# Performance work log

Measured on AMD Instinct MI355X. Metric: run time of the kernel, lower is better.

## Reference

```python
import jax, jax.numpy as jnp
import numpy as np

UP = 2
NUM_POINT = 9
GROUPS = 4


def pixel_shuffle(t, r):
    # [B, C*r*r, H, W] -> [B, C, H*r, W*r], torch layout: in[b, c*r*r + i*r + j, h, w] -> out[b, c, h*r+i, w*r+j]
    B, C, H, W = t.shape
    Co = C // (r * r)
    t = t.reshape(B, Co, r, r, H, W)
    t = t.transpose(0, 1, 4, 2, 5, 3)
    return t.reshape(B, Co, H * r, W * r)


def _bilinear_sample(feat, py, px):
    # feat: [E, H, W]; py, px: [P, Hup, Wup] in low-res pixel coords (zero padding outside)
    H, W = feat.shape[1], feat.shape[2]
    y0f = jnp.floor(py)
    x0f = jnp.floor(px)
    ty = py - y0f
    tx = px - x0f
    y0 = y0f.astype(jnp.int32)
    x0 = x0f.astype(jnp.int32)
    out = jnp.zeros(feat.shape[:1] + py.shape, dtype=feat.dtype)
    corners = ((0, 0, (1 - ty) * (1 - tx)), (0, 1, (1 - ty) * tx),
               (1, 0, ty * (1 - tx)), (1, 1, ty * tx))
    for dy, dx, w in corners:
        yi = y0 + dy
        xi = x0 + dx
        valid = ((yi >= 0) & (yi < H) & (xi >= 0) & (xi < W)).astype(feat.dtype)
        yc = jnp.clip(yi, 0, H - 1)
        xc = jnp.clip(xi, 0, W - 1)
        out = out + feat[:, yc, xc] * (w * valid)[None]
    return out  # [E, P, Hup, Wup]

# vmap over batch and group dims
_sample_bg = jax.vmap(jax.vmap(_bilinear_sample))


def setup_inputs() -> dict:
    key = jax.random.key(0)
    ks = jax.random.split(key, 8)
    B, Cy, Cx = 2, 256, 256
    H, W = 64, 64
    Hup, Wup = H * UP, W * UP
    GE = GROUPS * 32              # q/k channels = groups * embedding_dim
    OFF = GROUPS * NUM_POINT * 2 * UP * UP  # 288
    return {
        "y": jax.random.normal(ks[0], (B, Cy, Hup, Wup), jnp.float32),
        "x": jax.random.normal(ks[1], (B, Cx, H, W), jnp.float32),
        "Wq": jax.random.normal(ks[2], (GE, Cy), jnp.float32) * 0.02,
        "bq": jnp.zeros((GE,), jnp.float32),
        "Wk": jax.random.normal(ks[3], (GE, Cx), jnp.float32) * 0.02,
        "bk": jnp.zeros((GE,), jnp.float32),
        "Woff": jax.random.normal(ks[4], (OFF, Cx), jnp.float32) * 0.02,
        "boff": jnp.zeros((OFF,), jnp.float32),
    }


def reference(y, x, Wq, bq, Wk, bk, Woff, boff):
    G, P, up = GROUPS, NUM_POINT, UP
    B, C, H, W = x.shape
    # 1x1 convs as einsum
    q = jnp.einsum('oi,bihw->bohw', Wq, y) + bq[None, :, None, None]
    k = jnp.einsum('oi,bihw->bohw', Wk, x) + bk[None, :, None, None]
    off = jnp.einsum('oi,bihw->bohw', Woff, x) + boff[None, :, None, None]
    off = pixel_shuffle(off, up)  # [B, G*P*2, Hup, Wup]
    Hup, Wup = off.shape[2], off.shape[3]
    off = off.reshape(B, G, P, 2, Hup, Wup)
    # sampling positions in low-res coordinates: align-centers base + learned offset
    base_y = (jnp.arange(Hup, dtype=jnp.float32) + 0.5) / up - 0.5
    base_x = (jnp.arange(Wup, dtype=jnp.float32) + 0.5) / up - 0.5
    py = off[:, :, :, 0] + base_y[None, None, None, :, None]  # [B,G,P,Hup,Wup]
    px = off[:, :, :, 1] + base_x[None, None, None, None, :]
    E = Wq.shape[0] // G
    qg = q.reshape(B, G, E, Hup, Wup)
    kg = k.reshape(B, G, E, H, W)
    # deform_qk: gather k at offset points, dot with q over embedding dim
    ks = _sample_bg(kg, py, px)                    # [B,G,E,P,Hup,Wup]
    attn = jnp.einsum('bgehw,bgephw->bgphw', qg, ks)
    attn = jax.nn.softmax(attn, axis=2)            # softmax over points
    # deform_av: gather x at the same points, weighted sum by attn
    Cg = C // G
    xg = x.reshape(B, G, Cg, H, W)
    xs = _sample_bg(xg, py, px)                    # [B,G,Cg,P,Hup,Wup]
    out = jnp.einsum('bgphw,bgcphw->bgchw', attn, xs)
    return out.reshape(B, C, Hup, Wup)
```

## Files before the change

### kernel.cpp

```cpp
#include <hip/hip_runtime.h>

#define B_N   2
#define H_LR  64
#define W_LR  64
#define HUP   128
#define WUP   128
#define GRP   4
#define NPT   9
#define EMB   32
#define CGRP  64
#define KIN   256
#define GE    128
#define NOFF  288

typedef __attribute__((ext_vector_type(8))) short short8v;
typedef _Float16 half8v __attribute__((ext_vector_type(8)));
typedef __attribute__((ext_vector_type(4))) float f32x4;

__device__ __forceinline__ ushort f2bf(float f) {
    unsigned u = __float_as_uint(f);
    u += 0x7FFFu + ((u >> 16) & 1u);
    return (ushort)(u >> 16);
}
__device__ __forceinline__ float bf2f(ushort h) {
    return __uint_as_float(((unsigned)h) << 16);
}
__device__ __forceinline__ ushort f2h(float f) {
    _Float16 h = (_Float16)f;
    return __builtin_bit_cast(ushort, h);
}
__device__ __forceinline__ float h2f(ushort u) {
    _Float16 h = __builtin_bit_cast(_Float16, u);
    return (float)h;
}

__global__ __launch_bounds__(256) void convert_w_kernel(
    const float* __restrict__ Wq, const float* __restrict__ Wk,
    const float* __restrict__ Woff, ushort* __restrict__ wqbf,
    ushort* __restrict__ wkobf)
{
    int r = blockIdx.x, k = threadIdx.x;
    if (r < 128) {
        wqbf[r * 256 + k] = f2bf(Wq[r * 256 + k]);
    } else {
        int r2 = r - 128;
        float v = 0.f;
        if (r2 < 128) v = Wk[r2 * 256 + k];
        else if (r2 < 416) v = Woff[(r2 - 128) * 256 + k];
        wkobf[r2 * 256 + k] = f2bf(v);
    }
}

__global__ __launch_bounds__(256, 4) void mfma_gemm(
    const float* __restrict__ y, const float* __restrict__ x,
    const ushort* __restrict__ WQ, const ushort* __restrict__ WKO,
    const float* __restrict__ bq, const float* __restrict__ bk,
    const float* __restrict__ boff,
    ushort* __restrict__ qbf, ushort* __restrict__ kbf,
    float* __restrict__ offw)
{
    __shared__ __align__(16) ushort sY[64][68];
    __shared__ __align__(16) ushort sB[128][72];

    int bid = blockIdx.x;
    const float* SRC; const ushort* WBF; const float* ba; const float* bb;
    ushort* OBF; float* OFP;
    int M, m0, n0, b;
    if (bid < 512) {
        int mt = bid & 255; b = bid >> 8;
        SRC = y; WBF = WQ; ba = bq; bb = nullptr; OBF = qbf; OFP = nullptr;
        M = 16384; m0 = mt * 64; n0 = 0;
    } else {
        int r = bid - 512;
        int mt = r & 63, nt2 = (r >> 6) & 3; b = r >> 8;
        SRC = x; WBF = WKO; ba = bk; bb = boff; OBF = kbf; OFP = offw;
        M = 4096; m0 = mt * 64; n0 = nt2 * 128;
    }

    int tid = threadIdx.x;
    int lane = tid & 63;
    int wv = tid >> 6, wm = wv >> 1, wn = wv & 1;
    int il = lane & 15, g4 = lane >> 4;
    int st_m4 = tid & 15, st_c = tid >> 4;
    int st_c8 = tid & 7,  st_n = tid >> 3;

    f32x4 acc[2][4];
#pragma unroll
    for (int i = 0; i < 2; ++i)
#pragma unroll
        for (int j = 0; j < 4; ++j) { f32x4 z = {0.f,0.f,0.f,0.f}; acc[i][j] = z; }

    const float* src_b = SRC + (size_t)b * KIN * M;

    float4 ra[4]; short8v rb[4];
#pragma unroll
    for (int i = 0; i < 4; ++i)
        ra[i] = *(const float4*)&src_b[(size_t)(st_c + i * 16) * M + m0 + st_m4 * 4];
#pragma unroll
    for (int i = 0; i < 4; ++i)
        rb[i] = *(const short8v*)&WBF[(size_t)(n0 + st_n + i * 32) * KIN + st_c8 * 8];

    for (int ks = 0; ks < 4; ++ks) {
#pragma unroll
        for (int i = 0; i < 4; ++i) {
            ushort4 h;
            h.x = f2bf(ra[i].x); h.y = f2bf(ra[i].y);
            h.z = f2bf(ra[i].z); h.w = f2bf(ra[i].w);
            *(ushort4*)&sY[st_c + i * 16][st_m4 * 4] = h;
            *(short8v*)&sB[st_n + i * 32][st_c8 * 8] = rb[i];
        }
        __syncthreads();
        if (ks < 3) {
            int k0 = (ks + 1) * 64;
#pragma unroll
            for (int i = 0; i < 4; ++i)
                ra[i] = *(const float4*)&src_b[(size_t)(k0 + st_c + i * 16) * M + m0 + st_m4 * 4];
#pragma unroll
            for (int i = 0; i < 4; ++i)
                rb[i] = *(const short8v*)&WBF[(size_t)(n0 + st_n + i * 32) * KIN + k0 + st_c8 * 8];
        }
#pragma unroll
        for (int kc = 0; kc < 2; ++kc) {
            int kb = kc * 32 + g4 * 8;
            short8v af[2], bfr[4];
#pragma unroll
            for (int mf = 0; mf < 2; ++mf) {
                int m = wm * 32 + mf * 16 + il;
                short8v t;
#pragma unroll
                for (int j = 0; j < 8; ++j) t[j] = (short)sY[kb + j][m];
                af[mf] = t;
            }
#pragma unroll
            for (int nf = 0; nf < 4; ++nf)
                bfr[nf] = *(const short8v*)&sB[wn * 64 + nf * 16 + il][kb];
#pragma unroll
            for (int mf = 0; mf < 2; ++mf)
#pragma unroll
                for (int nf = 0; nf < 4; ++nf)
                    acc[mf][nf] = __builtin_amdgcn_mfma_f32_16x16x32_bf16(
                        af[mf], bfr[nf], acc[mf][nf], 0, 0, 0);
        }
        __syncthreads();
    }

#pragma unroll
    for (int mf = 0; mf < 2; ++mf) {
#pragma unroll
        for (int r = 0; r < 4; ++r) {
            int m = m0 + wm * 32 + mf * 16 + g4 * 4 + r;
            size_t row = (size_t)b * M + m;
#pragma unroll
            for (int nf = 0; nf < 4; ++nf) {
                int n = n0 + wn * 64 + nf * 16 + il;
                float v = acc[mf][nf][r];
                if (n < GE) {
                    OBF[row * 128 + n] = f2bf(v + ba[n]);
                } else {
                    int no = n - GE;
                    if (no < NOFF) OFP[row * 288 + no] = v + bb[no];
                }
            }
        }
    }
}

#define RROWS 6
#define RCOLS 11
#define RPX   66

__global__ __launch_bounds__(256, 4) void deform_kernel(
    const ushort* __restrict__ qbf,
    const ushort* __restrict__ kbf,
    const float* __restrict__ offw,
    const float* __restrict__ x,
    float* __restrict__ out)
{
    __shared__ __align__(16) char smem[36272];
    ushort (*sXt)[72] = (ushort(*)[72])(smem);
    ushort (*sK)[40]  = (ushort(*)[40])(smem + 9216);
    ushort (*sQ)[40]  = (ushort(*)[40])(smem + 14496);
    ushort (*sSW)[72] = (ushort(*)[72])(smem + 19616);
    uint*  sGt        = (uint*)(smem + 28832);
    int*   sGz        = (int*)(smem + 31136);
    float* sAttn      = (float*)(smem + 33440);
    int*   sFB        = (int*)(smem + 35744);
    float (*sOT)[76]  = (float(*)[76])(smem);
    float* sOff       = (float*)(smem + 19616);

    int bx = blockIdx.x;
    int tw = bx & 7, th = (bx >> 3) & 31, g = (bx >> 8) & 3, b = bx >> 10;
    int tid = threadIdx.x;
    int wv_ = tid >> 6, lane = tid & 63;
    int row = lane & 15, kb8 = lane >> 4;

    const int ry0 = th * 2 - 2, rx0 = tw * 8 - 1;

    if (tid == 0) sFB[0] = 0;
    if (tid < 192) {
        int r = tid / 3, c2 = tid - (tid / 3) * 3;
        *(uint*)&sXt[r][66 + c2 * 2] = 0;
    }
    for (int it = tid; it < 1536; it += 256) {
        int quad = it & 3, rest = it >> 2;
        int ch = rest / 6, gy = rest - (rest / 6) * 6;
        int gyg = min(max(ry0 + gy, 0), 63);
        const float* xr = x + ((size_t)b * 256 + g * CGRP + ch) * 4096 + gyg * 64;
        if (tw >= 1 && tw <= 6) {
            float4 f = *(const float4*)&xr[rx0 - 3 + quad * 4];
            const float* fv = (const float*)&f;
#pragma unroll
            for (int j = 0; j < 4; ++j) {
                int col = quad * 4 + j - 3;
                if (col >= 0 && col < RCOLS) sXt[ch][gy * RCOLS + col] = f2h(fv[j]);
            }
        } else {
#pragma unroll
            for (int j = 0; j < 4; ++j) {
                int col = quad * 4 + j - 3;
                if (col >= 0 && col < RCOLS) {
                    int gxg = min(max(rx0 + col, 0), 63);
                    sXt[ch][gy * RCOLS + col] = f2h(xr[gxg]);
                }
            }
        }
    }
    for (int i = tid; i < 264; i += 256) {
        int rp = i >> 2, c4 = i & 3;
        int qy = rp / RCOLS, qx = rp - qy * RCOLS;
        int gy = min(max(ry0 + qy, 0), 63), gx = min(max(rx0 + qx, 0), 63);
        *(short8v*)&sK[rp][c4 * 8] =
            *(const short8v*)&kbf[((size_t)b * 4096 + gy * 64 + gx) * 128 +
                                  g * EMB + c4 * 8];
    }
    {
        int px = tid >> 2, c4 = tid & 3;
        int hup = th * 4 + (px >> 4), wup = tw * 16 + (px & 15);
        *(short8v*)&sQ[px][c4 * 8] =
            *(const short8v*)&qbf[((size_t)b * 16384 + hup * 128 + wup) * 128 +
                                  g * EMB + c4 * 8];
    }
    for (int i = tid; i < 288; i += 256) {
        int lr = i / 18, f4 = i - (i / 18) * 18;
        int yy = th * 2 + (lr >> 3), xx = tw * 8 + (lr & 7);
        *(float4*)&sOff[lr * 72 + f4 * 4] =
            *(const float4*)&offw[((size_t)b * 4096 + yy * 64 + xx) * 288 +
                                  g * 72 + f4 * 4];
    }
    __syncthreads();

    f32x4 sreg[5];
    {
        short8v a = *(const short8v*)&sQ[wv_ * 16 + row][kb8 * 8];
#pragma unroll
        for (int nt = 0; nt < 5; ++nt) {
            int rr = nt * 16 + row; if (rr > 65) rr = 65;
            short8v bf = *(const short8v*)&sK[rr][kb8 * 8];
            f32x4 z = {0.f, 0.f, 0.f, 0.f};
            sreg[nt] = __builtin_amdgcn_mfma_f32_16x16x32_bf16(a, bf, z, 0, 0, 0);
        }
    }
    for (int item = tid; item < 576; item += 256) {
        int px = item / 9, pt = item - (item / 9) * 9;
        int lx = px & 15, ly = px >> 4;
        int hup = th * 4 + ly, wup = tw * 16 + lx;
        int lr = (ly >> 1) * 8 + (lx >> 1);
        int ij = ((hup & 1) << 1) | (wup & 1);
        float offy = sOff[lr * 72 + pt * 8 + ij];
        float offx = sOff[lr * 72 + pt * 8 + 4 + ij];
        float py  = offy + hup * 0.5f - 0.25f;
        float pxx = offx + wup * 0.5f - 0.25f;
        float y0f = floorf(py), x0f = floorf(pxx);
        float ty = py - y0f, tx = pxx - x0f;
        int y0 = (int)y0f, x0 = (int)x0f;
        int mk = 0;
        if ((unsigned)y0 < 64u && (unsigned)x0 < 64u)         mk |= 1;
        if ((unsigned)y0 < 64u && (unsigned)(x0+1) < 64u)     mk |= 2;
        if ((unsigned)(y0+1) < 64u && (unsigned)x0 < 64u)     mk |= 4;
        if ((unsigned)(y0+1) < 64u && (unsigned)(x0+1) < 64u) mk |= 8;
        int iy = y0 - ry0, ix = x0 - rx0;
        bool inreg = ((unsigned)iy <= (unsigned)(RROWS - 2)) &&
                     ((unsigned)ix <= (unsigned)(RCOLS - 2));
        int fl, zp;
        if (!mk)        { fl = 16; zp = 0; }
        else if (inreg) { fl = mk | 16; zp = iy * RCOLS + ix; }
        else            { fl = mk; zp = (y0 + 1) * 66 + (x0 + 1); }
        sGt[item] = (uint)f2h(ty) | ((uint)f2h(tx) << 16);
        sGz[item] = (zp << 5) | fl;
    }
    __syncthreads();

#pragma unroll
    for (int nt = 0; nt < 5; ++nt) {
        int rp = nt * 16 + row;
        if (rp < RPX) {
#pragma unroll
            for (int r = 0; r < 4; ++r)
                sSW[wv_ * 16 + kb8 * 4 + r][rp] = f2h(sreg[nt][r]);
        }
    }
    __syncthreads();

    for (int item = tid; item < 576; item += 256) {
        int px = item / 9;
        uint gt = sGt[item];
        float ty = h2f((ushort)gt), tx = h2f((ushort)(gt >> 16));
        int z = sGz[item];
        int fl = z & 31;
        float a;
        if (fl & 16) {
            int zi = z >> 5;
            float w00 = (1.f - ty) * (1.f - tx), w01 = (1.f - ty) * tx;
            float w10 = ty * (1.f - tx), w11 = ty * tx;
            a  = (fl & 1) ? w00 * h2f(sSW[px][zi])             : 0.f;
            a += (fl & 2) ? w01 * h2f(sSW[px][zi + 1])         : 0.f;
            a += (fl & 4) ? w10 * h2f(sSW[px][zi + RCOLS])     : 0.f;
            a += (fl & 8) ? w11 * h2f(sSW[px][zi + RCOLS + 1]) : 0.f;
        } else {
            int t = z >> 5;
            int y0 = t / 66 - 1, x0 = t - (t / 66) * 66 - 1;
            a = 0.f;
#pragma unroll
            for (int c = 0; c < 4; ++c) if ((fl >> c) & 1) {
                int dy = c >> 1, dx = c & 1;
                float wgt = (dy ? ty : 1.f - ty) * (dx ? tx : 1.f - tx);
                const ushort* kr = &kbf[((size_t)b * 4096 + (y0 + dy) * 64 + x0 + dx) * 128 +
                                        g * EMB];
                float dot = 0.f;
                for (int e = 0; e < EMB; ++e) dot += bf2f(sQ[px][e]) * bf2f(kr[e]);
                a += wgt * dot;
            }
            int old = atomicAdd(&sFB[0], 1);
            if (old < 128) sFB[1 + old] = item;
        }
        sAttn[item] = a;
    }
    __syncthreads();

    if (tid < 64) {
        float aa[NPT];
        float mx = -1e30f;
#pragma unroll
        for (int p = 0; p < NPT; ++p) { aa[p] = sAttn[tid * 9 + p]; mx = fmaxf(mx, aa[p]); }
        float s = 0.f;
#pragma unroll
        for (int p = 0; p < NPT; ++p) { aa[p] = __expf(aa[p] - mx); s += aa[p]; }
        float inv = 1.f / s;
#pragma unroll
        for (int p = 0; p < NPT; ++p) sAttn[tid * 9 + p] = aa[p] * inv;
    } else {
        float4* p = (float4*)&sSW[0][0];
        float4 z4 = make_float4(0.f, 0.f, 0.f, 0.f);
        for (int i = tid - 64; i < 576; i += 192) p[i] = z4;
    }
    __syncthreads();

    if (tid < 64) {
        int px = tid;
#pragma unroll
        for (int pt = 0; pt < NPT; ++pt) {
            int item = px * 9 + pt;
            int z = sGz[item];
            int fl = z & 31;
            if (!(fl & 16)) continue;
            uint gt = sGt[item];
            float ty = h2f((ushort)gt), tx = h2f((ushort)(gt >> 16));
            float a = sAttn[item];
            int zi = z >> 5;
            ushort* c = &sSW[px][zi];
            if (fl & 1) c[0]         = f2h(h2f(c[0])         + (1.f-ty)*(1.f-tx)*a);
            if (fl & 2) c[1]         = f2h(h2f(c[1])         + (1.f-ty)*tx*a);
            if (fl & 4) c[RCOLS]     = f2h(h2f(c[RCOLS])     + ty*(1.f-tx)*a);
            if (fl & 8) c[RCOLS + 1] = f2h(h2f(c[RCOLS + 1]) + ty*tx*a);
        }
    }
    __syncthreads();

    f32x4 oacc[4];
    {
        half8v bfm0[4], bfm1[4], bfm2[4];
#pragma unroll
        for (int nt = 0; nt < 4; ++nt) {
            bfm0[nt] = *(const half8v*)&sXt[nt * 16 + row][kb8 * 8];
            bfm1[nt] = *(const half8v*)&sXt[nt * 16 + row][32 + kb8 * 8];
            bfm2[nt] = *(const half8v*)&sXt[nt * 16 + row][64];
        }
        int px = wv_ * 16 + row;
        half8v af0 = *(const half8v*)&sSW[px][kb8 * 8];
        half8v af1 = *(const half8v*)&sSW[px][32 + kb8 * 8];
        half8v af2 = {0,0,0,0,0,0,0,0};
        if (kb8 == 0) af2 = *(const half8v*)&sSW[px][64];

#pragma unroll
        for (int nt = 0; nt < 4; ++nt) { f32x4 z = {0.f,0.f,0.f,0.f}; oacc[nt] = z; }
#pragma unroll
        for (int nt = 0; nt < 4; ++nt) {
            oacc[nt] = __builtin_amdgcn_mfma_f32_16x16x32_f16(af0, bfm0[nt], oacc[nt], 0, 0, 0);
            oacc[nt] = __builtin_amdgcn_mfma_f32_16x16x32_f16(af1, bfm1[nt], oacc[nt], 0, 0, 0);
            oacc[nt] = __builtin_amdgcn_mfma_f32_16x16x32_f16(af2, bfm2[nt], oacc[nt], 0, 0, 0);
        }
    }
    __syncthreads();

#pragma unroll
    for (int nt = 0; nt < 4; ++nt)
        *(f32x4*)&sOT[nt * 16 + row][wv_ * 16 + kb8 * 4] = oacc[nt];
    __syncthreads();

    {
#pragma unroll
        for (int i = 0; i < 4; ++i) {
            int pr = i * 64 + (tid >> 2);
            int ch = pr >> 2, hupl = pr & 3, q = tid & 3;
            float4 v = *(float4*)&sOT[ch][hupl * 16 + q * 4];
            *(float4*)(out + ((size_t)b * 256 + g * CGRP + ch) * 16384 +
                       (size_t)(th * 4 + hupl) * 128 + tw * 16 + q * 4) = v;
        }
    }
    __syncthreads();

    int nfb = min(sFB[0], 128);
    for (int i = 0; i < nfb; ++i) {
        if (tid < 64) {
            int item = sFB[1 + i];
            int px = item / 9;
            uint gt = sGt[item];
            float ty = h2f((ushort)gt), tx = h2f((ushort)(gt >> 16));
            int z = sGz[item];
            float a = sAttn[item];
            int fl = z & 15;
            int t = z >> 5;
            int y0 = t / 66 - 1, x0 = t - (t / 66) * 66 - 1;
            const float* xg = x + ((size_t)b * 256 + g * CGRP + tid) * 4096;
            float v = 0.f;
            if (fl & 1) v += (1.f-ty)*(1.f-tx)*a * xg[y0*64 + x0];
            if (fl & 2) v += (1.f-ty)*tx*a       * xg[y0*64 + x0 + 1];
            if (fl & 4) v += ty*(1.f-tx)*a       * xg[(y0+1)*64 + x0];
            if (fl & 8) v += ty*tx*a             * xg[(y0+1)*64 + x0 + 1];
            int hup = th * 4 + (px >> 4), wup = tw * 16 + (px & 15);
            float* op = out + ((size_t)b * 256 + g * CGRP + tid) * 16384 +
                        hup * 128 + wup;
            *op += v;
        }
    }
}

extern "C" void kernel_launch(void* const* d_in, const int* in_sizes, int n_in,
                              void* d_out, int out_size, void* d_ws, size_t ws_size,
                              hipStream_t stream)
{
    const float* y    = (const float*)d_in[0];
    const float* x    = (const float*)d_in[1];
    const float* Wq   = (const float*)d_in[2];
    const float* bq   = (const float*)d_in[3];
    const float* Wk   = (const float*)d_in[4];
    const float* bk   = (const float*)d_in[5];
    const float* Woff = (const float*)d_in[6];
    const float* boff = (const float*)d_in[7];
    float* out = (float*)d_out;

    ushort* wqbf  = (ushort*)d_ws;
    ushort* wkobf = wqbf + 128 * 256;
    ushort* qbf   = wkobf + 512 * 256;
    ushort* kbf   = qbf + (size_t)B_N * 16384 * 128;
    float*  offw  = (float*)(kbf + (size_t)B_N * 4096 * 128);

    convert_w_kernel<<<dim3(640), dim3(256), 0, stream>>>(Wq, Wk, Woff, wqbf, wkobf);

    mfma_gemm<<<dim3(1024), dim3(256), 0, stream>>>(
        y, x, wqbf, wkobf, bq, bk, boff, qbf, kbf, offw);

    deform_kernel<<<dim3(2048), dim3(256), 0, stream>>>(qbf, kbf, offw, x, out);
}
```

Before: 71.37 us.

## Fuse attention gather, softmax and scatter into one per-pixel pass

The deform kernel now writes the QK MFMA scores straight to shared memory instead of holding them in registers. One thread per pixel then gathers the scores, runs the softmax and scatters the bilinear weights in a single pass. This removes the separate attention buffer and several block barriers, and the fallback list now stores the softmax weight with each item. The final barrier is skipped when no out-of-region samples occur. In exchange, the attention work runs on one wave instead of all four, and the fallback list capacity drops from 128 to 64 entries.

```diff
diff --git a/kernel.cpp b/kernel.cpp
--- a/kernel.cpp
+++ b/kernel.cpp
@@ -176,17 +176,17 @@
     const float* __restrict__ x,
     float* __restrict__ out)
 {
-    __shared__ __align__(16) char smem[36272];
+    __shared__ __align__(16) char smem[37808];
     ushort (*sXt)[72] = (ushort(*)[72])(smem);
-    ushort (*sK)[40]  = (ushort(*)[40])(smem + 9216);
-    ushort (*sQ)[40]  = (ushort(*)[40])(smem + 14496);
-    ushort (*sSW)[72] = (ushort(*)[72])(smem + 19616);
-    uint*  sGt        = (uint*)(smem + 28832);
-    int*   sGz        = (int*)(smem + 31136);
-    float* sAttn      = (float*)(smem + 33440);
-    int*   sFB        = (int*)(smem + 35744);
-    float (*sOT)[76]  = (float(*)[76])(smem);
-    float* sOff       = (float*)(smem + 19616);
+    ushort (*sS)[66]  = (ushort(*)[66])(smem + 9216);
+    uint*  sGt        = (uint*)(smem + 17664);
+    int*   sGz        = (int*)(smem + 19968);
+    int*   sFB        = (int*)(smem + 22272);
+    ushort (*sQ)[40]  = (ushort(*)[40])(smem + 22800);
+    ushort (*sK)[40]  = (ushort(*)[40])(smem + 27920);
+    float* sOff       = (float*)(smem + 33200);
+    ushort (*sW)[72]  = (ushort(*)[72])(smem + 27920);
+    float (*sOT)[68]  = (float(*)[68])(smem);
 
     int bx = blockIdx.x;
     int tw = bx & 7, th = (bx >> 3) & 31, g = (bx >> 8) & 3, b = bx >> 10;
@@ -249,7 +249,6 @@
     }
     __syncthreads();
 
-    f32x4 sreg[5];
     {
         short8v a = *(const short8v*)&sQ[wv_ * 16 + row][kb8 * 8];
 #pragma unroll
@@ -257,7 +256,13 @@
             int rr = nt * 16 + row; if (rr > 65) rr = 65;
             short8v bf = *(const short8v*)&sK[rr][kb8 * 8];
             f32x4 z = {0.f, 0.f, 0.f, 0.f};
-            sreg[nt] = __builtin_amdgcn_mfma_f32_16x16x32_bf16(a, bf, z, 0, 0, 0);
+            f32x4 d = __builtin_amdgcn_mfma_f32_16x16x32_bf16(a, bf, z, 0, 0, 0);
+            int rp = nt * 16 + row;
+            if (rp < RPX) {
+#pragma unroll
+                for (int r = 0; r < 4; ++r)
+                    sS[wv_ * 16 + kb8 * 4 + r][rp] = f2h(d[r]);
+            }
         }
     }
     for (int item = tid; item < 576; item += 256) {
@@ -290,88 +295,81 @@
     }
     __syncthreads();
 
-#pragma unroll
-    for (int nt = 0; nt < 5; ++nt) {
-        int rp = nt * 16 + row;
-        if (rp < RPX) {
-#pragma unroll
-            for (int r = 0; r < 4; ++r)
-                sSW[wv_ * 16 + kb8 * 4 + r][rp] = f2h(sreg[nt][r]);
-        }
-    }
-    __syncthreads();
-
-    for (int item = tid; item < 576; item += 256) {
-        int px = item / 9;
-        uint gt = sGt[item];
-        float ty = h2f((ushort)gt), tx = h2f((ushort)(gt >> 16));
-        int z = sGz[item];
-        int fl = z & 31;
-        float a;
-        if (fl & 16) {
-            int zi = z >> 5;
-            float w00 = (1.f - ty) * (1.f - tx), w01 = (1.f - ty) * tx;
-            float w10 = ty * (1.f - tx), w11 = ty * tx;
-            a  = (fl & 1) ? w00 * h2f(sSW[px][zi])             : 0.f;
-            a += (fl & 2) ? w01 * h2f(sSW[px][zi + 1])         : 0.f;
-            a += (fl & 4) ? w10 * h2f(sSW[px][zi + RCOLS])     : 0.f;
-            a += (fl & 8) ? w11 * h2f(sSW[px][zi + RCOLS + 1]) : 0.f;
-        } else {
-            int t = z >> 5;
-            int y0 = t / 66 - 1, x0 = t - (t / 66) * 66 - 1;
-            a = 0.f;
-#pragma unroll
-            for (int c = 0; c < 4; ++c) if ((fl >> c) & 1) {
-                int dy = c >> 1, dx = c & 1;
-                float wgt = (dy ? ty : 1.f - ty) * (dx ? tx : 1.f - tx);
-                const ushort* kr = &kbf[((size_t)b * 4096 + (y0 + dy) * 64 + x0 + dx) * 128 +
-                                        g * EMB];
-                float dot = 0.f;
-                for (int e = 0; e < EMB; ++e) dot += bf2f(sQ[px][e]) * bf2f(kr[e]);
-                a += wgt * dot;
-            }
-            int old = atomicAdd(&sFB[0], 1);
-            if (old < 128) sFB[1 + old] = item;
-        }
-        sAttn[item] = a;
-    }
-    __syncthreads();
-
     if (tid < 64) {
-        float aa[NPT];
-        float mx = -1e30f;
-#pragma unroll
-        for (int p = 0; p < NPT; ++p) { aa[p] = sAttn[tid * 9 + p]; mx = fmaxf(mx, aa[p]); }
+        int px = tid;
+        float aa[NPT], ty9[NPT], tx9[NPT];
+        int gz9[NPT];
+#pragma unroll
+        for (int p = 0; p < NPT; ++p) {
+            int item = px * 9 + p;
+            uint gt = sGt[item];
+            ty9[p] = h2f((ushort)gt); tx9[p] = h2f((ushort)(gt >> 16));
+            gz9[p] = sGz[item];
+        }
+#pragma unroll
+        for (int p = 0; p < NPT; ++p) {
+            int z = gz9[p];
+            int fl = z & 31;
+            float ty = ty9[p], tx = tx9[p];
+            float a;
+            if (fl & 16) {
+                int zi = z >> 5;
+                float w00 = (1.f - ty) * (1.f - tx), w01 = (1.f - ty) * tx;
+                float w10 = ty * (1.f - tx), w11 = ty * tx;
+                a  = (fl & 1) ? w00 * h2f(sS[px][zi])             : 0.f;
+                a += (fl & 2) ? w01 * h2f(sS[px][zi + 1])         : 0.f;
+                a += (fl & 4) ? w10 * h2f(sS[px][zi + RCOLS])     : 0.f;
+                a += (fl & 8) ? w11 * h2f(sS[px][zi + RCOLS + 1]) : 0.f;
+            } else {
+                int t = z >> 5;
+                int y0 = t / 66 - 1, x0 = t - (t / 66) * 66 - 1;
+                a = 0.f;
+#pragma unroll
+                for (int c = 0; c < 4; ++c) if ((fl >> c) & 1) {
+                    int dy = c >> 1, dx = c & 1;
+                    float wgt = (dy ? ty : 1.f - ty) * (dx ? tx : 1.f - tx);
+                    const ushort* kr = &kbf[((size_t)b * 4096 + (y0 + dy) * 64 + x0 + dx) * 128 +
+                                            g * EMB];
+                    float dot = 0.f;
+                    for (int e = 0; e < EMB; ++e) dot += bf2f(sQ[px][e]) * bf2f(kr[e]);
+                    a += wgt * dot;
+                }
+            }
+            aa[p] = a;
+        }
+        float mx = aa[0];
+#pragma unroll
+        for (int p = 1; p < NPT; ++p) mx = fmaxf(mx, aa[p]);
         float s = 0.f;
 #pragma unroll
         for (int p = 0; p < NPT; ++p) { aa[p] = __expf(aa[p] - mx); s += aa[p]; }
         float inv = 1.f / s;
-#pragma unroll
-        for (int p = 0; p < NPT; ++p) sAttn[tid * 9 + p] = aa[p] * inv;
-    } else {
-        float4* p = (float4*)&sSW[0][0];
-        float4 z4 = make_float4(0.f, 0.f, 0.f, 0.f);
-        for (int i = tid - 64; i < 576; i += 192) p[i] = z4;
-    }
-    __syncthreads();
-
-    if (tid < 64) {
-        int px = tid;
-#pragma unroll
-        for (int pt = 0; pt < NPT; ++pt) {
-            int item = px * 9 + pt;
-            int z = sGz[item];
+        {
+            float4 z4 = make_float4(0.f, 0.f, 0.f, 0.f);
+            char* wr = (char*)&sW[px][0];
+#pragma unroll
+            for (int j = 0; j < 9; ++j) *(float4*)(wr + j * 16) = z4;
+        }
+#pragma unroll
+        for (int p = 0; p < NPT; ++p) {
+            float a = aa[p] * inv;
+            int z = gz9[p];
             int fl = z & 31;
-            if (!(fl & 16)) continue;
-            uint gt = sGt[item];
-            float ty = h2f((ushort)gt), tx = h2f((ushort)(gt >> 16));
-            float a = sAttn[item];
-            int zi = z >> 5;
-            ushort* c = &sSW[px][zi];
-            if (fl & 1) c[0]         = f2h(h2f(c[0])         + (1.f-ty)*(1.f-tx)*a);
-            if (fl & 2) c[1]         = f2h(h2f(c[1])         + (1.f-ty)*tx*a);
-            if (fl & 4) c[RCOLS]     = f2h(h2f(c[RCOLS])     + ty*(1.f-tx)*a);
-            if (fl & 8) c[RCOLS + 1] = f2h(h2f(c[RCOLS + 1]) + ty*tx*a);
+            if (fl & 16) {
+                float ty = ty9[p], tx = tx9[p];
+                int zi = z >> 5;
+                ushort* c = &sW[px][zi];
+                if (fl & 1) c[0]         = f2h(h2f(c[0])         + (1.f-ty)*(1.f-tx)*a);
+                if (fl & 2) c[1]         = f2h(h2f(c[1])         + (1.f-ty)*tx*a);
+                if (fl & 4) c[RCOLS]     = f2h(h2f(c[RCOLS])     + ty*(1.f-tx)*a);
+                if (fl & 8) c[RCOLS + 1] = f2h(h2f(c[RCOLS + 1]) + ty*tx*a);
+            } else {
+                int old = atomicAdd(&sFB[0], 1);
+                if (old < 64) {
+                    sFB[1 + 2 * old] = px * 9 + p;
+                    sFB[2 + 2 * old] = __float_as_int(a);
+                }
+            }
         }
     }
     __syncthreads();
@@ -386,10 +384,10 @@
             bfm2[nt] = *(const half8v*)&sXt[nt * 16 + row][64];
         }
         int px = wv_ * 16 + row;
-        half8v af0 = *(const half8v*)&sSW[px][kb8 * 8];
-        half8v af1 = *(const half8v*)&sSW[px][32 + kb8 * 8];
+        half8v af0 = *(const half8v*)&sW[px][kb8 * 8];
+        half8v af1 = *(const half8v*)&sW[px][32 + kb8 * 8];
         half8v af2 = {0,0,0,0,0,0,0,0};
-        if (kb8 == 0) af2 = *(const half8v*)&sSW[px][64];
+        if (kb8 == 0) af2 = *(const half8v*)&sW[px][64];
 
 #pragma unroll
         for (int nt = 0; nt < 4; ++nt) { f32x4 z = {0.f,0.f,0.f,0.f}; oacc[nt] = z; }
@@ -407,40 +405,40 @@
         *(f32x4*)&sOT[nt * 16 + row][wv_ * 16 + kb8 * 4] = oacc[nt];
     __syncthreads();
 
-    {
-#pragma unroll
-        for (int i = 0; i < 4; ++i) {
-            int pr = i * 64 + (tid >> 2);
-            int ch = pr >> 2, hupl = pr & 3, q = tid & 3;
-            float4 v = *(float4*)&sOT[ch][hupl * 16 + q * 4];
-            *(float4*)(out + ((size_t)b * 256 + g * CGRP + ch) * 16384 +
-                       (size_t)(th * 4 + hupl) * 128 + tw * 16 + q * 4) = v;
-        }
-    }
-    __syncthreads();
-
-    int nfb = min(sFB[0], 128);
-    for (int i = 0; i < nfb; ++i) {
-        if (tid < 64) {
-            int item = sFB[1 + i];
-            int px = item / 9;
-            uint gt = sGt[item];
-            float ty = h2f((ushort)gt), tx = h2f((ushort)(gt >> 16));
-            int z = sGz[item];
-            float a = sAttn[item];
-            int fl = z & 15;
-            int t = z >> 5;
-            int y0 = t / 66 - 1, x0 = t - (t / 66) * 66 - 1;
-            const float* xg = x + ((size_t)b * 256 + g * CGRP + tid) * 4096;
-            float v = 0.f;
-            if (fl & 1) v += (1.f-ty)*(1.f-tx)*a * xg[y0*64 + x0];
-            if (fl & 2) v += (1.f-ty)*tx*a       * xg[y0*64 + x0 + 1];
-            if (fl & 4) v += ty*(1.f-tx)*a       * xg[(y0+1)*64 + x0];
-            if (fl & 8) v += ty*tx*a             * xg[(y0+1)*64 + x0 + 1];
-            int hup = th * 4 + (px >> 4), wup = tw * 16 + (px & 15);
-            float* op = out + ((size_t)b * 256 + g * CGRP + tid) * 16384 +
-                        hup * 128 + wup;
-            *op += v;
+#pragma unroll
+    for (int i = 0; i < 4; ++i) {
+        int pr = i * 64 + (tid >> 2);
+        int ch = pr >> 2, hupl = pr & 3, q = tid & 3;
+        float4 v = *(float4*)&sOT[ch][hupl * 16 + q * 4];
+        *(float4*)(out + ((size_t)b * 256 + g * CGRP + ch) * 16384 +
+                   (size_t)(th * 4 + hupl) * 128 + tw * 16 + q * 4) = v;
+    }
+
+    int nfb = min(sFB[0], 64);
+    if (nfb > 0) {
+        __syncthreads();
+        for (int i = 0; i < nfb; ++i) {
+            if (tid < 64) {
+                int item = sFB[1 + 2 * i];
+                float a  = __int_as_float(sFB[2 + 2 * i]);
+                int px = item / 9;
+                uint gt = sGt[item];
+                float ty = h2f((ushort)gt), tx = h2f((ushort)(gt >> 16));
+                int z = sGz[item];
+                int fl = z & 15;
+                int t = z >> 5;
+                int y0 = t / 66 - 1, x0 = t - (t / 66) * 66 - 1;
+                const float* xg = x + ((size_t)b * 256 + g * CGRP + tid) * 4096;
+                float v = 0.f;
+                if (fl & 1) v += (1.f-ty)*(1.f-tx)*a * xg[y0*64 + x0];
+                if (fl & 2) v += (1.f-ty)*tx*a       * xg[y0*64 + x0 + 1];
+                if (fl & 4) v += ty*(1.f-tx)*a       * xg[(y0+1)*64 + x0];
+                if (fl & 8) v += ty*tx*a             * xg[(y0+1)*64 + x0 + 1];
+                int hup = th * 4 + (px >> 4), wup = tw * 16 + (px & 15);
+                float* op = out + ((size_t)b * 256 + g * CGRP + tid) * 16384 +
+                            hup * 128 + wup;
+                *op += v;
+            }
         }
     }
 }
```

Result: slower. 74.78 us (+4.8%).
